# Kernel optimization log

Hardware: AMD Instinct MI355X
Metric: run time of the kernel (lower is better)

The kernel has to match this reference:

```python
import jax, jax.numpy as jnp
import numpy as np


def setup_inputs() -> dict:
    key = jax.random.key(0)
    k1, k2 = jax.random.split(key)
    B, N, M = 4, 8192, 8192
    pred = jax.random.normal(k1, (B, N, 3), dtype=jnp.float32)
    target = jax.random.normal(k2, (B, M, 3), dtype=jnp.float32)
    return {"pred": pred, "target": target}


def reference(pred, target):
    # pairwise L1 distance matrix: [B, N, M]
    dist = jnp.abs(pred[:, :, None, :] - target[:, None, :, :]).sum(axis=-1)
    forward_dist = dist.min(axis=2)   # [B, N] nearest target for each pred point
    backward_dist = dist.min(axis=1)  # [B, M] nearest pred for each target point
    per_batch = forward_dist.sum(axis=1) + backward_dist.sum(axis=1)  # [B]
    B = pred.shape[0]
    return per_batch.sum() / B  # reduction='mean'
```

## Files before the change

### kernel.cpp

```cpp
#include <hip/hip_runtime.h>
#include <stdint.h>


#define BATCH    4
#define NPTS     8192
#define QSCALE   4096.0f
#define QOFFS    8.0f
#define NP       8
#define NT       4
#define NPTS_TOT (2 * BATCH * NPTS)

static __device__ __forceinline__ uint32_t sad_u16(uint32_t a, uint32_t b, uint32_t c) {
#if __has_builtin(__builtin_amdgcn_sad_u16)
    return __builtin_amdgcn_sad_u16(a, b, c);
#else
    uint32_t d;
    asm("v_sad_u16 %0, %1, %2, %3" : "=v"(d) : "v"(a), "v"(b), "v"(c));
    return d;
#endif
}

static __device__ __forceinline__ uint32_t min3_u32(uint32_t a, uint32_t b, uint32_t c) {
    uint32_t d;
    asm("v_min3_u32 %0, %1, %2, %3" : "=v"(d) : "v"(a), "v"(b), "v"(c));
    return d;
}

static __device__ __forceinline__ uint32_t umin32(uint32_t a, uint32_t b) {
    return a < b ? a : b;
}

static __device__ __forceinline__ uint32_t rot16(uint32_t v) {
    return (uint32_t)__builtin_amdgcn_update_dpp((int)v, (int)v, 0x121, 0xF, 0xF, false);
}

static __device__ __forceinline__ uint32_t quant(float x) {
    float v = (x + QOFFS) * QSCALE;
    v = fminf(fmaxf(v, 0.0f), 65535.0f);
    return (uint32_t)(v + 0.5f);
}


__global__ __launch_bounds__(256) void chamfer_prep_kernel(
    const float* __restrict__ pred, const float* __restrict__ target,
    uint32_t* __restrict__ wsmin, uint2* __restrict__ wsq,
    float* __restrict__ out)
{
    const int tid = blockIdx.x * 256 + threadIdx.x;
    if (tid == 0) out[0] = 0.0f;
    wsmin[tid] = 0xFFFFFFFFu;
    const float* src = (tid < NPTS_TOT / 2)
                     ? pred + (size_t)tid * 3
                     : target + (size_t)(tid - NPTS_TOT / 2) * 3;
    wsq[tid] = make_uint2(quant(src[0]) | (quant(src[1]) << 16), quant(src[2]));
}

__global__ __launch_bounds__(256, 8) void chamfer_sym_kernel(
    const uint2* __restrict__ wsq, uint32_t* __restrict__ wsmin)
{
    const int t    = threadIdx.x;
    const int wid  = t >> 6;
    const int lane = t & 63;
    const int g16  = lane >> 4;
    const int l16  = lane & 15;

    const int tid    = blockIdx.x * 4 + wid;
    const int b      = tid >> 11;
    const int rest   = tid & 2047;
    const int pblock = rest >> 5;
    const int tblock = rest & 31;

    const int pb = pblock * 128;
    const int tb = tblock * 256;
    const uint2* qsrc = wsq + (size_t)b * NPTS;
    const uint2* tsrc = wsq + (size_t)(BATCH + b) * NPTS;

    uint32_t qxy[NP], qz[NP], rowacc[NP];
    #pragma unroll
    for (int k = 0; k < NP; ++k) {
        uint2 v = qsrc[pb + k * 16 + l16];
        qxy[k] = v.x;  qz[k] = v.y;  rowacc[k] = 0xFFFFFFFFu;
    }

    uint32_t txy[NT], tz[NT], colacc[NT];
    #pragma unroll
    for (int m = 0; m < NT; ++m) {
        uint2 v = tsrc[tb + g16 * 64 + m * 16 + l16];
        txy[m] = v.x;  tz[m] = v.y;  colacc[m] = 0xFFFFFFFFu;
    }

    #pragma unroll 4
    for (int r = 0; r < 16; ++r) {
        #pragma unroll
        for (int kk = 0; kk < NP; kk += 2) {
            uint32_t d0[NT], d1[NT];
            #pragma unroll
            for (int m = 0; m < NT; ++m) {
                d0[m] = sad_u16(tz[m], qz[kk],     sad_u16(txy[m], qxy[kk],     0u));
                d1[m] = sad_u16(tz[m], qz[kk + 1], sad_u16(txy[m], qxy[kk + 1], 0u));
            }
            rowacc[kk]     = min3_u32(d0[0], d0[1], min3_u32(d0[2], d0[3], rowacc[kk]));
            rowacc[kk + 1] = min3_u32(d1[0], d1[1], min3_u32(d1[2], d1[3], rowacc[kk + 1]));
            #pragma unroll
            for (int m = 0; m < NT; ++m)
                colacc[m] = min3_u32(d0[m], d1[m], colacc[m]);
        }
        #pragma unroll
        for (int m = 0; m < NT; ++m) {
            txy[m]    = rot16(txy[m]);
            tz[m]     = rot16(tz[m]);
            colacc[m] = rot16(colacc[m]);
        }
    }

    uint32_t* fmin = wsmin + (size_t)b * NPTS;
    #pragma unroll
    for (int k = 0; k < NP; ++k) {
        uint32_t v = rowacc[k];
        v = umin32(v, (uint32_t)__shfl_xor((int)v, 16));
        v = umin32(v, (uint32_t)__shfl_xor((int)v, 32));
        if (g16 == 0)
            atomicMin(&fmin[pb + k * 16 + l16], v);
    }

    uint32_t* bmin = wsmin + (size_t)(BATCH + b) * NPTS;
    #pragma unroll
    for (int m = 0; m < NT; ++m)
        atomicMin(&bmin[tb + g16 * 64 + m * 16 + l16], colacc[m]);
}

__global__ __launch_bounds__(256) void chamfer_reduce_kernel(
    const uint32_t* __restrict__ wsmin, float* __restrict__ out)
{
    const int t = threadIdx.x;
    const uint4* p = reinterpret_cast<const uint4*>(wsmin);
    float s = 0.0f;
    #pragma unroll
    for (int i = 0; i < 4; ++i) {
        uint4 v = p[blockIdx.x * 1024 + i * 256 + t];
        s += (float)v.x + (float)v.y + (float)v.z + (float)v.w;
    }
    #pragma unroll
    for (int off = 32; off > 0; off >>= 1)
        s += __shfl_down(s, off);
    if ((t & 63) == 0)
        atomicAdd(out, s * (1.0f / (QSCALE * (float)BATCH)));
}

extern "C" void kernel_launch(void* const* d_in, const int* in_sizes, int n_in,
                              void* d_out, int out_size, void* d_ws, size_t ws_size,
                              hipStream_t stream) {
    const float* pred   = (const float*)d_in[0];
    const float* target = (const float*)d_in[1];
    float* out = (float*)d_out;
    uint32_t* wsmin = (uint32_t*)d_ws;
    uint2*    wsq   = (uint2*)((char*)d_ws + 256 * 1024);

    chamfer_prep_kernel<<<NPTS_TOT / 256, 256, 0, stream>>>(pred, target, wsmin, wsq, out);

    chamfer_sym_kernel<<<2048, 256, 0, stream>>>(wsq, wsmin);

    chamfer_reduce_kernel<<<16, 256, 0, stream>>>(wsmin, out);
}
```

Measured before the change: 37.84 us.

## Fuse quantization into main kernel and fold final reduction via last-block counter

Quantization of the point coordinates moves into the main symmetric kernel, which now reads the float inputs directly. The separate reduce kernel is replaced by a last-block-done pattern: an atomic counter picks the final block, which sums all minima and writes the output. Inline-asm min3 is also replaced with plain min chains that the compiler can fuse. This drops one kernel launch and the quantized workspace round trip, at the cost of each block re-quantizing its points, strided float loads, and a serial reduction in a single block at the tail.

```diff
diff --git a/kernel.cpp b/kernel.cpp
--- a/kernel.cpp
+++ b/kernel.cpp
@@ -8,7 +8,7 @@
 #define QOFFS    8.0f
 #define NP       8
 #define NT       4
-#define NPTS_TOT (2 * BATCH * NPTS)
+#define NBLK     2048
 
 static __device__ __forceinline__ uint32_t sad_u16(uint32_t a, uint32_t b, uint32_t c) {
 #if __has_builtin(__builtin_amdgcn_sad_u16)
@@ -18,12 +18,6 @@
     asm("v_sad_u16 %0, %1, %2, %3" : "=v"(d) : "v"(a), "v"(b), "v"(c));
     return d;
 #endif
-}
-
-static __device__ __forceinline__ uint32_t min3_u32(uint32_t a, uint32_t b, uint32_t c) {
-    uint32_t d;
-    asm("v_min3_u32 %0, %1, %2, %3" : "=v"(d) : "v"(a), "v"(b), "v"(c));
-    return d;
 }
 
 static __device__ __forceinline__ uint32_t umin32(uint32_t a, uint32_t b) {
@@ -41,22 +35,18 @@
 }
 
 
-__global__ __launch_bounds__(256) void chamfer_prep_kernel(
-    const float* __restrict__ pred, const float* __restrict__ target,
-    uint32_t* __restrict__ wsmin, uint2* __restrict__ wsq,
-    float* __restrict__ out)
+__global__ __launch_bounds__(256) void chamfer_init_kernel(
+    uint32_t* __restrict__ wsmin, uint32_t* __restrict__ counter)
 {
     const int tid = blockIdx.x * 256 + threadIdx.x;
-    if (tid == 0) out[0] = 0.0f;
     wsmin[tid] = 0xFFFFFFFFu;
-    const float* src = (tid < NPTS_TOT / 2)
-                     ? pred + (size_t)tid * 3
-                     : target + (size_t)(tid - NPTS_TOT / 2) * 3;
-    wsq[tid] = make_uint2(quant(src[0]) | (quant(src[1]) << 16), quant(src[2]));
+    if (tid == 0) *counter = 0;
 }
 
 __global__ __launch_bounds__(256, 8) void chamfer_sym_kernel(
-    const uint2* __restrict__ wsq, uint32_t* __restrict__ wsmin)
+    const float* __restrict__ pred, const float* __restrict__ target,
+    uint32_t* __restrict__ wsmin, uint32_t* __restrict__ counter,
+    float* __restrict__ out)
 {
     const int t    = threadIdx.x;
     const int wid  = t >> 6;
@@ -72,21 +62,25 @@
 
     const int pb = pblock * 128;
     const int tb = tblock * 256;
-    const uint2* qsrc = wsq + (size_t)b * NPTS;
-    const uint2* tsrc = wsq + (size_t)(BATCH + b) * NPTS;
+    const float* qsrc = pred   + (size_t)b * NPTS * 3;
+    const float* tsrc = target + (size_t)b * NPTS * 3;
 
     uint32_t qxy[NP], qz[NP], rowacc[NP];
     #pragma unroll
     for (int k = 0; k < NP; ++k) {
-        uint2 v = qsrc[pb + k * 16 + l16];
-        qxy[k] = v.x;  qz[k] = v.y;  rowacc[k] = 0xFFFFFFFFu;
+        const float* p = qsrc + (size_t)(pb + k * 16 + l16) * 3;
+        qxy[k] = quant(p[0]) | (quant(p[1]) << 16);
+        qz[k]  = quant(p[2]);
+        rowacc[k] = 0xFFFFFFFFu;
     }
 
     uint32_t txy[NT], tz[NT], colacc[NT];
     #pragma unroll
     for (int m = 0; m < NT; ++m) {
-        uint2 v = tsrc[tb + g16 * 64 + m * 16 + l16];
-        txy[m] = v.x;  tz[m] = v.y;  colacc[m] = 0xFFFFFFFFu;
+        const float* p = tsrc + (size_t)(tb + g16 * 64 + m * 16 + l16) * 3;
+        txy[m] = quant(p[0]) | (quant(p[1]) << 16);
+        tz[m]  = quant(p[2]);
+        colacc[m] = 0xFFFFFFFFu;
     }
 
     #pragma unroll 4
@@ -99,11 +93,11 @@
                 d0[m] = sad_u16(tz[m], qz[kk],     sad_u16(txy[m], qxy[kk],     0u));
                 d1[m] = sad_u16(tz[m], qz[kk + 1], sad_u16(txy[m], qxy[kk + 1], 0u));
             }
-            rowacc[kk]     = min3_u32(d0[0], d0[1], min3_u32(d0[2], d0[3], rowacc[kk]));
-            rowacc[kk + 1] = min3_u32(d1[0], d1[1], min3_u32(d1[2], d1[3], rowacc[kk + 1]));
+            rowacc[kk]     = umin32(umin32(umin32(d0[0], d0[1]), umin32(d0[2], d0[3])), rowacc[kk]);
+            rowacc[kk + 1] = umin32(umin32(umin32(d1[0], d1[1]), umin32(d1[2], d1[3])), rowacc[kk + 1]);
             #pragma unroll
             for (int m = 0; m < NT; ++m)
-                colacc[m] = min3_u32(d0[m], d1[m], colacc[m]);
+                colacc[m] = umin32(umin32(d0[m], d1[m]), colacc[m]);
         }
         #pragma unroll
         for (int m = 0; m < NT; ++m) {
@@ -127,24 +121,31 @@
     #pragma unroll
     for (int m = 0; m < NT; ++m)
         atomicMin(&bmin[tb + g16 * 64 + m * 16 + l16], colacc[m]);
-}
 
-__global__ __launch_bounds__(256) void chamfer_reduce_kernel(
-    const uint32_t* __restrict__ wsmin, float* __restrict__ out)
-{
-    const int t = threadIdx.x;
+    __shared__ float ssum[4];
+    __shared__ uint32_t lastflag;
+    __threadfence();
+    if (t == 0)
+        lastflag = (atomicAdd(counter, 1u) == NBLK - 1);
+    __syncthreads();
+    if (!lastflag) return;
+    __threadfence();
+
     const uint4* p = reinterpret_cast<const uint4*>(wsmin);
     float s = 0.0f;
     #pragma unroll
-    for (int i = 0; i < 4; ++i) {
-        uint4 v = p[blockIdx.x * 1024 + i * 256 + t];
+    for (int i = 0; i < 64; ++i) {
+        uint4 v = p[t + i * 256];
         s += (float)v.x + (float)v.y + (float)v.z + (float)v.w;
     }
     #pragma unroll
     for (int off = 32; off > 0; off >>= 1)
         s += __shfl_down(s, off);
-    if ((t & 63) == 0)
-        atomicAdd(out, s * (1.0f / (QSCALE * (float)BATCH)));
+    if (lane == 0) ssum[wid] = s;
+    __syncthreads();
+    if (t == 0)
+        out[0] = (ssum[0] + ssum[1] + ssum[2] + ssum[3])
+               * (1.0f / (QSCALE * (float)BATCH));
 }
 
 extern "C" void kernel_launch(void* const* d_in, const int* in_sizes, int n_in,
@@ -153,12 +154,9 @@
     const float* pred   = (const float*)d_in[0];
     const float* target = (const float*)d_in[1];
     float* out = (float*)d_out;
-    uint32_t* wsmin = (uint32_t*)d_ws;
-    uint2*    wsq   = (uint2*)((char*)d_ws + 256 * 1024);
+    uint32_t* wsmin   = (uint32_t*)d_ws;
+    uint32_t* counter = (uint32_t*)((char*)d_ws + 256 * 1024);
 
-    chamfer_prep_kernel<<<NPTS_TOT / 256, 256, 0, stream>>>(pred, target, wsmin, wsq, out);
-
-    chamfer_sym_kernel<<<2048, 256, 0, stream>>>(wsq, wsmin);
-
-    chamfer_reduce_kernel<<<16, 256, 0, stream>>>(wsmin, out);
+    chamfer_init_kernel<<<256, 256, 0, stream>>>(wsmin, counter);
+    chamfer_sym_kernel<<<NBLK, 256, 0, stream>>>(pred, target, wsmin, counter, out);
 }
```

New measurement: 145.2 us. 284% more time.

## Replace global atomicMin with per-slot partial minima and slot-reducing pass

Applied to the files above, without the earlier changes.

The symmetric kernel now writes each tile's row and column partial minima to dedicated slots (32 forward slots, 64 backward slots) with plain stores instead of atomicMin into a shared buffer. The reduce kernel takes the minimum across slots before summing, and runs with more blocks. This removes atomic contention and the initialization writes from the prep kernel. In exchange it adds about 12 MB of workspace writes and reads (4 MB forward, 8 MB backward) in the reduce pass.

```diff
diff --git a/kernel.cpp b/kernel.cpp
--- a/kernel.cpp
+++ b/kernel.cpp
@@ -9,6 +9,9 @@
 #define NP       8
 #define NT       4
 #define NPTS_TOT (2 * BATCH * NPTS)
+#define BN       (BATCH * NPTS)
+#define SLOTF    32
+#define SLOTB    64
 
 static __device__ __forceinline__ uint32_t sad_u16(uint32_t a, uint32_t b, uint32_t c) {
 #if __has_builtin(__builtin_amdgcn_sad_u16)
@@ -43,12 +46,10 @@
 
 __global__ __launch_bounds__(256) void chamfer_prep_kernel(
     const float* __restrict__ pred, const float* __restrict__ target,
-    uint32_t* __restrict__ wsmin, uint2* __restrict__ wsq,
-    float* __restrict__ out)
+    uint2* __restrict__ wsq, float* __restrict__ out)
 {
     const int tid = blockIdx.x * 256 + threadIdx.x;
     if (tid == 0) out[0] = 0.0f;
-    wsmin[tid] = 0xFFFFFFFFu;
     const float* src = (tid < NPTS_TOT / 2)
                      ? pred + (size_t)tid * 3
                      : target + (size_t)(tid - NPTS_TOT / 2) * 3;
@@ -56,7 +57,8 @@
 }
 
 __global__ __launch_bounds__(256, 8) void chamfer_sym_kernel(
-    const uint2* __restrict__ wsq, uint32_t* __restrict__ wsmin)
+    const uint2* __restrict__ wsq,
+    uint32_t* __restrict__ wsf, uint32_t* __restrict__ wsb)
 {
     const int t    = threadIdx.x;
     const int wid  = t >> 6;
@@ -113,38 +115,44 @@
         }
     }
 
-    uint32_t* fmin = wsmin + (size_t)b * NPTS;
+    uint32_t* fslot = wsf + (size_t)tblock * BN + (size_t)b * NPTS;
     #pragma unroll
     for (int k = 0; k < NP; ++k) {
         uint32_t v = rowacc[k];
         v = umin32(v, (uint32_t)__shfl_xor((int)v, 16));
         v = umin32(v, (uint32_t)__shfl_xor((int)v, 32));
         if (g16 == 0)
-            atomicMin(&fmin[pb + k * 16 + l16], v);
+            fslot[pb + k * 16 + l16] = v;
     }
 
-    uint32_t* bmin = wsmin + (size_t)(BATCH + b) * NPTS;
+    uint32_t* bslot = wsb + (size_t)pblock * BN + (size_t)b * NPTS;
     #pragma unroll
     for (int m = 0; m < NT; ++m)
-        atomicMin(&bmin[tb + g16 * 64 + m * 16 + l16], colacc[m]);
+        bslot[tb + g16 * 64 + m * 16 + l16] = colacc[m];
 }
 
 __global__ __launch_bounds__(256) void chamfer_reduce_kernel(
-    const uint32_t* __restrict__ wsmin, float* __restrict__ out)
+    const uint32_t* __restrict__ wsf, const uint32_t* __restrict__ wsb,
+    float* __restrict__ out)
 {
-    const int t = threadIdx.x;
-    const uint4* p = reinterpret_cast<const uint4*>(wsmin);
-    float s = 0.0f;
-    #pragma unroll
-    for (int i = 0; i < 4; ++i) {
-        uint4 v = p[blockIdx.x * 1024 + i * 256 + t];
-        s += (float)v.x + (float)v.y + (float)v.z + (float)v.w;
-    }
+    const int tid = blockIdx.x * 256 + threadIdx.x;
+
+    uint32_t mf = 0xFFFFFFFFu;
+    #pragma unroll 8
+    for (int s = 0; s < SLOTF; ++s)
+        mf = umin32(mf, wsf[(size_t)s * BN + tid]);
+
+    uint32_t mb = 0xFFFFFFFFu;
+    #pragma unroll 8
+    for (int s = 0; s < SLOTB; ++s)
+        mb = umin32(mb, wsb[(size_t)s * BN + tid]);
+
+    float fsum = (float)mf + (float)mb;
     #pragma unroll
     for (int off = 32; off > 0; off >>= 1)
-        s += __shfl_down(s, off);
-    if ((t & 63) == 0)
-        atomicAdd(out, s * (1.0f / (QSCALE * (float)BATCH)));
+        fsum += __shfl_down(fsum, off);
+    if ((threadIdx.x & 63) == 0)
+        atomicAdd(out, fsum * (1.0f / (QSCALE * (float)BATCH)));
 }
 
 extern "C" void kernel_launch(void* const* d_in, const int* in_sizes, int n_in,
@@ -153,12 +161,13 @@
     const float* pred   = (const float*)d_in[0];
     const float* target = (const float*)d_in[1];
     float* out = (float*)d_out;
-    uint32_t* wsmin = (uint32_t*)d_ws;
-    uint2*    wsq   = (uint2*)((char*)d_ws + 256 * 1024);
+    uint2*    wsq = (uint2*)d_ws;
+    uint32_t* wsf = (uint32_t*)((char*)d_ws + 512 * 1024);
+    uint32_t* wsb = (uint32_t*)((char*)d_ws + 512 * 1024 + 4 * 1024 * 1024);
 
-    chamfer_prep_kernel<<<NPTS_TOT / 256, 256, 0, stream>>>(pred, target, wsmin, wsq, out);
+    chamfer_prep_kernel<<<NPTS_TOT / 256, 256, 0, stream>>>(pred, target, wsq, out);
 
-    chamfer_sym_kernel<<<2048, 256, 0, stream>>>(wsq, wsmin);
+    chamfer_sym_kernel<<<2048, 256, 0, stream>>>(wsq, wsf, wsb);
 
-    chamfer_reduce_kernel<<<16, 256, 0, stream>>>(wsmin, out);
+    chamfer_reduce_kernel<<<128, 256, 0, stream>>>(wsf, wsb, out);
 }
```

Measured after the change: 50.03 us. +32.2%, slower.
